# Kernel optimization log

Hardware: AMD Instinct MI355X
Metric: run time of the kernel (lower is better)

## Reference

```python
import jax, jax.numpy as jnp
import numpy as np

WINDOW = 512  # window_size from init_kwargs


def _sliding_window_attn(q, k, v, window):
    # q,k,v: [B, S, H, D]; each query attends to keys j with i-window < j <= i (causal band)
    B, S, H, D = q.shape
    W = window
    NB = S // W  # S chosen divisible by W
    qb = q.reshape(B, NB, W, H, D)
    kb = k.reshape(B, NB, W, H, D)
    vb = v.reshape(B, NB, W, H, D)
    # previous block of keys/values (zeros for block 0, masked out below)
    kprev = jnp.pad(kb, ((0, 0), (1, 0), (0, 0), (0, 0), (0, 0)))[:, :NB]
    vprev = jnp.pad(vb, ((0, 0), (1, 0), (0, 0), (0, 0), (0, 0)))[:, :NB]
    kcat = jnp.concatenate([kprev, kb], axis=2)  # [B, NB, 2W, H, D]
    vcat = jnp.concatenate([vprev, vb], axis=2)
    qi = jnp.arange(W)
    kj = jnp.arange(2 * W) - W  # key position relative to block start
    rel = kj[None, :] - qi[:, None]  # [W, 2W]
    win_mask = (rel <= 0) & (rel > -W)  # causal window of size W (incl. self)
    blk = jnp.arange(NB)
    valid_key = (blk[:, None, None] > 0) | (kj[None, None, :] >= 0)  # block 0 has no prev
    mask = win_mask[None] & valid_key  # [NB, W, 2W]
    scale = 1.0 / np.sqrt(D).astype(np.float32)
    scores = jnp.einsum('bnqhd,bnkhd->bhnqk', qb, kcat) * scale  # [B,H,NB,W,2W]
    scores = jnp.where(mask[None, None], scores, jnp.finfo(scores.dtype).min)
    probs = jax.nn.softmax(scores, axis=-1)
    out = jnp.einsum('bhnqk,bnkhd->bnqhd', probs, vcat)  # [B,NB,W,H,D]
    return out.reshape(B, S, H, D)


def setup_inputs() -> dict:
    B, S, H, D = 2, 8192, 8, 64
    root = jax.random.key(0)
    k1, k2, k3, k4, k5 = jax.random.split(root, 5)
    query = jax.random.normal(k1, (B, S, H, D), dtype=jnp.float32)
    key = jax.random.normal(k2, (B, S, H, D), dtype=jnp.float32)
    value = jax.random.normal(k3, (B, S, H, D), dtype=jnp.float32)
    W_out = jax.random.normal(k4, (H * D, H * D), dtype=jnp.float32) * (1.0 / np.sqrt(H * D))
    b_out = jax.random.normal(k5, (H * D,), dtype=jnp.float32) * 0.01
    return {'query': query, 'key': key, 'value': value, 'W_out': W_out, 'b_out': b_out}


def reference(query, key, value, W_out, b_out):
    B, S, H, D = query.shape
    # seq_len (8192) > window_size (512) -> sliding-window branch of the module
    attn = _sliding_window_attn(query, key, value, WINDOW)
    flat = attn.reshape(B, S, H * D)
    # out_proj (nn.Linear); dropout=0.0 is identity; no attention_mask
    return flat @ W_out.T + b_out
```

## Files before the change

### kernel.cpp

```cpp
#include <hip/hip_runtime.h>

#define B_ 2
#define S_ 8192
#define H_ 8
#define D_ 64
#define HD_ 512
#define WIN_ 512

typedef __bf16 bf16x8 __attribute__((ext_vector_type(8)));
typedef float f32x4 __attribute__((ext_vector_type(4)));
typedef unsigned short u16;
typedef unsigned int u32;

__device__ __forceinline__ u16 f2bf(float f) {
  u32 u = __float_as_uint(f);
  u += 0x7FFFu + ((u >> 16) & 1u);
  return (u16)(u >> 16);
}

__device__ __forceinline__ bf16x8 cvt8s(const float* p, float s) {
  const float4 a = *(const float4*)p;
  const float4 b = *(const float4*)(p + 4);
  union { u16 s[8]; bf16x8 v; } r;
  r.s[0] = f2bf(a.x * s); r.s[1] = f2bf(a.y * s); r.s[2] = f2bf(a.z * s); r.s[3] = f2bf(a.w * s);
  r.s[4] = f2bf(b.x * s); r.s[5] = f2bf(b.y * s); r.s[6] = f2bf(b.z * s); r.s[7] = f2bf(b.w * s);
  return r.v;
}

#define MFMA(a, b, c) __builtin_amdgcn_mfma_f32_16x16x32_bf16(a, b, c, 0, 0, 0)

__global__ __launch_bounds__(256) void cvt_kernel(const float* __restrict__ in,
                                                  u16* __restrict__ out, int n4) {
  int i = blockIdx.x * 256 + threadIdx.x;
  if (i < n4) {
    float4 f = ((const float4*)in)[i];
    ushort4 r;
    r.x = f2bf(f.x); r.y = f2bf(f.y); r.z = f2bf(f.z); r.w = f2bf(f.w);
    ((ushort4*)out)[i] = r;
  }
}

__global__ __launch_bounds__(1024, 4) void attn_kernel(const float* __restrict__ q,
                                                       const float* __restrict__ kf,
                                                       const float* __restrict__ vf,
                                                       u16* __restrict__ attn) {
  const int tid = threadIdx.x;
  const int lane = tid & 63;
  const int wave = tid >> 6;
  const int lg = lane >> 4;
  const int lj = lane & 15;
  const int bid = (int)blockIdx.x;
  const int swz = (bid & 7) * 64 + (bid >> 3);
  const int qc = swz & 31;
  const int bh = swz >> 5;
  const int b = bh >> 3, h = bh & 7;
  const int q0blk = qc * 256;
  const int q0w = q0blk + wave * 16;

  __shared__ __align__(16) u16 klds0[64 * 64], klds1[64 * 64];
  __shared__ __align__(16) u16 vlds0[64 * 64], vlds1[64 * 64];
  __shared__ __align__(16) u16 plds[16][16 * 40];

  const float qscale = 0.125f * 1.4426950408889634f;
  bf16x8 aq0, aq1;
  {
    const float* qrow = q + ((size_t)(b * S_ + q0w + lj) * H_ + h) * D_;
    aq0 = cvt8s(qrow + lg * 8, qscale);
    aq1 = cvt8s(qrow + 32 + lg * 8, qscale);
  }

  f32x4 o0 = {0.f, 0.f, 0.f, 0.f}, o1 = o0, o2 = o0, o3 = o0;
  float lacc[4] = {0.f, 0.f, 0.f, 0.f};

  const int tbw32 = (q0w >= WIN_) ? ((q0w - (WIN_ - 1)) >> 5) : 0;
  const int tew32 = (q0w + 15) >> 5;
  const bool wmask = (q0w >= WIN_);
  const int tbu = (q0blk >= WIN_) ? ((q0blk - (WIN_ - 1)) >> 6) : 0;
  const int teu = (q0blk + 255) >> 6;

  const bool isK = (tid < 256);
  const bool stager = (tid < 512);
  const float *gfA = nullptr, *gfB = nullptr;
  const size_t gstepf = (size_t)64 * H_ * D_;
  int dstA = 0, dstB = 0, vkey = 0, vd0 = 0;
  if (isK) {
    const int c = tid & 7;
    const int r0 = tid >> 3;
    const int r1 = r0 + 32;
    gfA = kf + ((size_t)(b * S_ + r0) * H_ + h) * D_ + c * 8;
    gfB = kf + ((size_t)(b * S_ + r1) * H_ + h) * D_ + c * 8;
    dstA = r0 * 64 + ((c * 8) ^ ((r0 & 7) << 3));
    dstB = r1 * 64 + ((c * 8) ^ ((r1 & 7) << 3));
  } else if (stager) {
    const int u = tid - 256;
    vkey = u & 63;
    vd0 = (u >> 6) * 8;
    gfA = vf + ((size_t)(b * S_ + vkey) * H_ + h) * D_ + vd0;
    gfB = gfA + 32;
  }

  auto kpack = [](float4 a, float4 c) {
    union { u16 s[8]; uint4 q; } t;
    t.s[0] = f2bf(a.x); t.s[1] = f2bf(a.y); t.s[2] = f2bf(a.z); t.s[3] = f2bf(a.w);
    t.s[4] = f2bf(c.x); t.s[5] = f2bf(c.y); t.s[6] = f2bf(c.z); t.s[7] = f2bf(c.w);
    return t.q;
  };
  auto vscatter = [&](u16* vb, int d0, float4 a, float4 c) {
    float vals[8] = {a.x, a.y, a.z, a.w, c.x, c.y, c.z, c.w};
#pragma unroll
    for (int i = 0; i < 8; ++i) {
      const int d = d0 + i;
      vb[d * 64 + (vkey ^ ((d & 7) << 3))] = f2bf(vals[i]);
    }
  };

  const int ko0 = lj * 64 + ((lg * 8) ^ ((lj & 7) << 3));
  const int ko1 = lj * 64 + ((32 + lg * 8) ^ ((lj & 7) << 3));
  const int po = lj * 40 + lg * 8;

  if (stager) {
    float4 a0 = *(const float4*)(gfA + gstepf * tbu);
    float4 b0 = *(const float4*)(gfA + gstepf * tbu + 4);
    float4 a1 = *(const float4*)(gfB + gstepf * tbu);
    float4 b1 = *(const float4*)(gfB + gstepf * tbu + 4);
    if (isK) {
      *(uint4*)(klds0 + dstA) = kpack(a0, b0);
      *(uint4*)(klds0 + dstB) = kpack(a1, b1);
    } else {
      vscatter(vlds0, vd0, a0, b0);
      vscatter(vlds0, vd0 + 32, a1, b1);
    }
  }
  float4 gaA, gbA, gaB, gbB;
  if (stager && tbu < teu) {
    gaA = *(const float4*)(gfA + gstepf * (tbu + 1));
    gbA = *(const float4*)(gfA + gstepf * (tbu + 1) + 4);
    gaB = *(const float4*)(gfB + gstepf * (tbu + 1));
    gbB = *(const float4*)(gfB + gstepf * (tbu + 1) + 4);
  }
  __syncthreads();

  int cur = 0;
  for (int t = tbu; t <= teu; ++t) {
    const u16* K = cur ? klds1 : klds0;
    const u16* V = cur ? vlds1 : vlds0;
#pragma unroll
    for (int s = 0; s < 2; ++s) {
      const int ts = t * 2 + s;
      if (ts >= tbw32 && ts <= tew32) {
        const u16* Kb = K + s * 2048;
        bf16x8 k00 = *(const bf16x8*)(Kb + ko0);
        bf16x8 k01 = *(const bf16x8*)(Kb + ko1);
        bf16x8 k10 = *(const bf16x8*)(Kb + ko0 + 1024);
        bf16x8 k11 = *(const bf16x8*)(Kb + ko1 + 1024);

        f32x4 sA = {0.f, 0.f, 0.f, 0.f}, sB = sA;
        sA = MFMA(aq0, k00, sA);
        sA = MFMA(aq1, k01, sA);
        sB = MFMA(aq0, k10, sB);
        sB = MFMA(aq1, k11, sB);

        const bool edge = (ts == tew32) || (wmask && ts == tbw32);
        const int kt = ts * 32;
        u16* ps = &plds[wave][0];
#pragma unroll
        for (int r = 0; r < 4; ++r) {
          float ea = __builtin_amdgcn_exp2f(sA[r]);
          float eb = __builtin_amdgcn_exp2f(sB[r]);
          if (edge) {
            const int qpos = q0w + lg * 4 + r;
            const int kA = kt + lj, kB = kA + 16;
            const bool okA = (kA <= qpos) && (kA > qpos - WIN_);
            const bool okB = (kB <= qpos) && (kB > qpos - WIN_);
            ea = okA ? ea : 0.f;
            eb = okB ? eb : 0.f;
          }
          lacc[r] += ea + eb;
          ps[(lg * 4 + r) * 40 + lj] = (u16)(__float_as_uint(ea) >> 16);
          ps[(lg * 4 + r) * 40 + 16 + lj] = (u16)(__float_as_uint(eb) >> 16);
        }
        bf16x8 ap = *(const bf16x8*)(ps + po);

        const int vos = lj * 64 + ((s * 32 + lg * 8) ^ ((lj & 7) << 3));
        bf16x8 v0 = *(const bf16x8*)(V + vos);
        bf16x8 v1 = *(const bf16x8*)(V + vos + 1024);
        bf16x8 v2 = *(const bf16x8*)(V + vos + 2048);
        bf16x8 v3 = *(const bf16x8*)(V + vos + 3072);
        o0 = MFMA(ap, v0, o0);
        o1 = MFMA(ap, v1, o1);
        o2 = MFMA(ap, v2, o2);
        o3 = MFMA(ap, v3, o3);
      }
    }

    if (stager && t < teu) {
      if (isK) {
        u16* dl = cur ? klds0 : klds1;
        *(uint4*)(dl + dstA) = kpack(gaA, gbA);
        *(uint4*)(dl + dstB) = kpack(gaB, gbB);
      } else {
        u16* vb = cur ? vlds0 : vlds1;
        vscatter(vb, vd0, gaA, gbA);
        vscatter(vb, vd0 + 32, gaB, gbB);
      }
    }
    __syncthreads();
    if (stager && t + 1 < teu) {
      gaA = *(const float4*)(gfA + gstepf * (t + 2));
      gbA = *(const float4*)(gfA + gstepf * (t + 2) + 4);
      gaB = *(const float4*)(gfB + gstepf * (t + 2));
      gbB = *(const float4*)(gfB + gstepf * (t + 2) + 4);
    }
    cur ^= 1;
  }

#pragma unroll
  for (int r = 0; r < 4; ++r) {
    float l = lacc[r];
    l += __shfl_xor(l, 1);
    l += __shfl_xor(l, 2);
    l += __shfl_xor(l, 4);
    l += __shfl_xor(l, 8);
    const float inv = 1.0f / l;
    const int row = q0w + lg * 4 + r;
    u16* orow = attn + (size_t)(b * S_ + row) * HD_ + h * D_;
    orow[lj] = f2bf(o0[r] * inv);
    orow[16 + lj] = f2bf(o1[r] * inv);
    orow[32 + lj] = f2bf(o2[r] * inv);
    orow[48 + lj] = f2bf(o3[r] * inv);
  }
}

__global__ __launch_bounds__(512) void gemm_kernel(const u16* __restrict__ A,
                                                   const u16* __restrict__ Wb,
                                                   const float* __restrict__ bias,
                                                   float* __restrict__ out) {
  const int tid = threadIdx.x;
  const int lane = tid & 63;
  const int wave = tid >> 6;
  const int lg = lane >> 4, lj = lane & 15;
  const int phys = (int)blockIdx.x;
  const int swz = (phys & 7) * 32 + (phys >> 3);
  const int rb = swz >> 1, cb = swz & 1;
  const int wr = wave >> 2, wc = wave & 3;
  const int row0 = rb * 128;
  const int col0 = cb * 256 + wc * 64;

  __shared__ __align__(16) u16 alds[2][128 * 64];

  const int srow = tid >> 3;
  const int skc = tid & 7;
  const u16* ag0 = A + (size_t)(row0 + srow) * HD_ + skc * 8;
  const u16* ag1 = A + (size_t)(row0 + 64 + srow) * HD_ + skc * 8;
  const int dst0 = srow * 64 + ((skc * 8) ^ ((srow & 7) << 3));
  const int dst1 = (64 + srow) * 64 + ((skc * 8) ^ ((srow & 7) << 3));

  f32x4 acc[4][4];
#pragma unroll
  for (int fr = 0; fr < 4; ++fr)
#pragma unroll
    for (int fc = 0; fc < 4; ++fc) acc[fr][fc] = (f32x4){0.f, 0.f, 0.f, 0.f};

  *(uint4*)(&alds[0][dst0]) = *(const uint4*)ag0;
  *(uint4*)(&alds[0][dst1]) = *(const uint4*)ag1;
  __syncthreads();

  uint4 pre0, pre1;
  int cur = 0;
  for (int kt = 0; kt < HD_; kt += 64) {
    if (kt + 64 < HD_) {
      pre0 = *(const uint4*)(ag0 + kt + 64);
      pre1 = *(const uint4*)(ag1 + kt + 64);
    }
    const u16* Abuf = alds[cur];
#pragma unroll
    for (int ks = 0; ks < 2; ++ks) {
      bf16x8 fa[4], fb[4];
#pragma unroll
      for (int fr = 0; fr < 4; ++fr) {
        const int rr = wr * 64 + fr * 16 + lj;
        fa[fr] = *(const bf16x8*)(Abuf + rr * 64 + ((ks * 32 + lg * 8) ^ ((lj & 7) << 3)));
      }
#pragma unroll
      for (int fc = 0; fc < 4; ++fc)
        fb[fc] = *(const bf16x8*)(Wb + (size_t)(col0 + fc * 16 + lj) * HD_ + kt + ks * 32 + lg * 8);
#pragma unroll
      for (int fr = 0; fr < 4; ++fr)
#pragma unroll
        for (int fc = 0; fc < 4; ++fc)
          acc[fr][fc] = MFMA(fa[fr], fb[fc], acc[fr][fc]);
    }
    if (kt + 64 < HD_) {
      u16* db = alds[cur ^ 1];
      *(uint4*)(&db[dst0]) = pre0;
      *(uint4*)(&db[dst1]) = pre1;
    }
    __syncthreads();
    cur ^= 1;
  }

#pragma unroll
  for (int fc = 0; fc < 4; ++fc) {
    const float bv = bias[col0 + fc * 16 + lj];
#pragma unroll
    for (int fr = 0; fr < 4; ++fr) {
#pragma unroll
      for (int r = 0; r < 4; ++r) {
        const int row = row0 + wr * 64 + fr * 16 + lg * 4 + r;
        out[(size_t)row * HD_ + col0 + fc * 16 + lj] = acc[fr][fc][r] + bv;
      }
    }
  }
}

extern "C" void kernel_launch(void* const* d_in, const int* in_sizes, int n_in,
                              void* d_out, int out_size, void* d_ws, size_t ws_size,
                              hipStream_t stream) {
  const float* q = (const float*)d_in[0];
  const float* k = (const float*)d_in[1];
  const float* v = (const float*)d_in[2];
  const float* w = (const float*)d_in[3];
  const float* bias = (const float*)d_in[4];
  float* out = (float*)d_out;

  char* ws = (char*)d_ws;
  u16* attn = (u16*)ws;
  u16* wb = (u16*)(ws + 16777216);

  hipLaunchKernelGGL(cvt_kernel, dim3(256), dim3(256), 0, stream, w, wb, 65536);
  hipLaunchKernelGGL(attn_kernel, dim3(512), dim3(1024), 0, stream, q, k, v, attn);
  hipLaunchKernelGGL(gemm_kernel, dim3(256), dim3(512), 0, stream, attn, wb, bias, out);
}
```

Baseline: 83.94 us.

## Process two 16-row query sub-tiles per wave to reuse K/V fragments

Each wave now handles 32 query rows as two 16-row sub-tiles, and each block covers 512 queries instead of 256, so the grid is halved. K and V fragments loaded from LDS are reused across both sub-tiles, which cuts LDS traffic and the global K/V staging per query. Costs are more registers per thread (two sets of accumulators and Q fragments), fewer blocks (256) to fill the GPU, and some extra wasted tiles at the window edges.

```diff
diff --git a/kernel.cpp b/kernel.cpp
--- a/kernel.cpp
+++ b/kernel.cpp
@@ -50,33 +50,44 @@
   const int lg = lane >> 4;
   const int lj = lane & 15;
   const int bid = (int)blockIdx.x;
-  const int swz = (bid & 7) * 64 + (bid >> 3);
-  const int qc = swz & 31;
-  const int bh = swz >> 5;
+  const int swz = (bid & 7) * 32 + (bid >> 3);
+  const int qc = swz & 15;
+  const int bh = swz >> 4;
   const int b = bh >> 3, h = bh & 7;
-  const int q0blk = qc * 256;
-  const int q0w = q0blk + wave * 16;
+  const int q0blk = qc * 512;
+  const int q0w = q0blk + wave * 32;
 
   __shared__ __align__(16) u16 klds0[64 * 64], klds1[64 * 64];
   __shared__ __align__(16) u16 vlds0[64 * 64], vlds1[64 * 64];
   __shared__ __align__(16) u16 plds[16][16 * 40];
 
   const float qscale = 0.125f * 1.4426950408889634f;
-  bf16x8 aq0, aq1;
-  {
-    const float* qrow = q + ((size_t)(b * S_ + q0w + lj) * H_ + h) * D_;
-    aq0 = cvt8s(qrow + lg * 8, qscale);
-    aq1 = cvt8s(qrow + 32 + lg * 8, qscale);
-  }
-
-  f32x4 o0 = {0.f, 0.f, 0.f, 0.f}, o1 = o0, o2 = o0, o3 = o0;
-  float lacc[4] = {0.f, 0.f, 0.f, 0.f};
-
-  const int tbw32 = (q0w >= WIN_) ? ((q0w - (WIN_ - 1)) >> 5) : 0;
-  const int tew32 = (q0w + 15) >> 5;
-  const bool wmask = (q0w >= WIN_);
+  bf16x8 aq[2][2];
+#pragma unroll
+  for (int qs = 0; qs < 2; ++qs) {
+    const float* qrow = q + ((size_t)(b * S_ + q0w + qs * 16 + lj) * H_ + h) * D_;
+    aq[qs][0] = cvt8s(qrow + lg * 8, qscale);
+    aq[qs][1] = cvt8s(qrow + 32 + lg * 8, qscale);
+  }
+
+  f32x4 o[2][4];
+#pragma unroll
+  for (int qs = 0; qs < 2; ++qs)
+#pragma unroll
+    for (int g = 0; g < 4; ++g) o[qs][g] = (f32x4){0.f, 0.f, 0.f, 0.f};
+  float lacc[2][4] = {};
+
+  const int ts_end = q0w >> 5;
+  int tbq[2];
+  bool wm[2];
+#pragma unroll
+  for (int qs = 0; qs < 2; ++qs) {
+    const int qq = q0w + qs * 16;
+    wm[qs] = (qq >= WIN_);
+    tbq[qs] = wm[qs] ? ((qq - (WIN_ - 1)) >> 5) : 0;
+  }
   const int tbu = (q0blk >= WIN_) ? ((q0blk - (WIN_ - 1)) >> 6) : 0;
-  const int teu = (q0blk + 255) >> 6;
+  const int teu = (q0blk + 511) >> 6;
 
   const bool isK = (tid < 256);
   const bool stager = (tid < 512);
@@ -147,49 +158,52 @@
 #pragma unroll
     for (int s = 0; s < 2; ++s) {
       const int ts = t * 2 + s;
-      if (ts >= tbw32 && ts <= tew32) {
+      if (ts >= tbq[0] && ts <= ts_end) {
         const u16* Kb = K + s * 2048;
         bf16x8 k00 = *(const bf16x8*)(Kb + ko0);
         bf16x8 k01 = *(const bf16x8*)(Kb + ko1);
         bf16x8 k10 = *(const bf16x8*)(Kb + ko0 + 1024);
         bf16x8 k11 = *(const bf16x8*)(Kb + ko1 + 1024);
-
-        f32x4 sA = {0.f, 0.f, 0.f, 0.f}, sB = sA;
-        sA = MFMA(aq0, k00, sA);
-        sA = MFMA(aq1, k01, sA);
-        sB = MFMA(aq0, k10, sB);
-        sB = MFMA(aq1, k11, sB);
-
-        const bool edge = (ts == tew32) || (wmask && ts == tbw32);
-        const int kt = ts * 32;
-        u16* ps = &plds[wave][0];
-#pragma unroll
-        for (int r = 0; r < 4; ++r) {
-          float ea = __builtin_amdgcn_exp2f(sA[r]);
-          float eb = __builtin_amdgcn_exp2f(sB[r]);
-          if (edge) {
-            const int qpos = q0w + lg * 4 + r;
-            const int kA = kt + lj, kB = kA + 16;
-            const bool okA = (kA <= qpos) && (kA > qpos - WIN_);
-            const bool okB = (kB <= qpos) && (kB > qpos - WIN_);
-            ea = okA ? ea : 0.f;
-            eb = okB ? eb : 0.f;
-          }
-          lacc[r] += ea + eb;
-          ps[(lg * 4 + r) * 40 + lj] = (u16)(__float_as_uint(ea) >> 16);
-          ps[(lg * 4 + r) * 40 + 16 + lj] = (u16)(__float_as_uint(eb) >> 16);
-        }
-        bf16x8 ap = *(const bf16x8*)(ps + po);
-
         const int vos = lj * 64 + ((s * 32 + lg * 8) ^ ((lj & 7) << 3));
         bf16x8 v0 = *(const bf16x8*)(V + vos);
         bf16x8 v1 = *(const bf16x8*)(V + vos + 1024);
         bf16x8 v2 = *(const bf16x8*)(V + vos + 2048);
         bf16x8 v3 = *(const bf16x8*)(V + vos + 3072);
-        o0 = MFMA(ap, v0, o0);
-        o1 = MFMA(ap, v1, o1);
-        o2 = MFMA(ap, v2, o2);
-        o3 = MFMA(ap, v3, o3);
+
+        const int kt = ts * 32;
+#pragma unroll
+        for (int qs = 0; qs < 2; ++qs) {
+          if (ts < tbq[qs]) continue;
+          f32x4 sA = {0.f, 0.f, 0.f, 0.f}, sB = sA;
+          sA = MFMA(aq[qs][0], k00, sA);
+          sA = MFMA(aq[qs][1], k01, sA);
+          sB = MFMA(aq[qs][0], k10, sB);
+          sB = MFMA(aq[qs][1], k11, sB);
+
+          const bool edge = (ts == ts_end) || (wm[qs] && ts == tbq[qs]);
+          u16* ps = &plds[wave][0];
+#pragma unroll
+          for (int r = 0; r < 4; ++r) {
+            float ea = __builtin_amdgcn_exp2f(sA[r]);
+            float eb = __builtin_amdgcn_exp2f(sB[r]);
+            if (edge) {
+              const int qpos = q0w + qs * 16 + lg * 4 + r;
+              const int kA = kt + lj, kB = kA + 16;
+              const bool okA = (kA <= qpos) && (kA > qpos - WIN_);
+              const bool okB = (kB <= qpos) && (kB > qpos - WIN_);
+              ea = okA ? ea : 0.f;
+              eb = okB ? eb : 0.f;
+            }
+            lacc[qs][r] += ea + eb;
+            ps[(lg * 4 + r) * 40 + lj] = (u16)(__float_as_uint(ea) >> 16);
+            ps[(lg * 4 + r) * 40 + 16 + lj] = (u16)(__float_as_uint(eb) >> 16);
+          }
+          bf16x8 ap = *(const bf16x8*)(ps + po);
+          o[qs][0] = MFMA(ap, v0, o[qs][0]);
+          o[qs][1] = MFMA(ap, v1, o[qs][1]);
+          o[qs][2] = MFMA(ap, v2, o[qs][2]);
+          o[qs][3] = MFMA(ap, v3, o[qs][3]);
+        }
       }
     }
 
@@ -215,19 +229,22 @@
   }
 
 #pragma unroll
-  for (int r = 0; r < 4; ++r) {
-    float l = lacc[r];
-    l += __shfl_xor(l, 1);
-    l += __shfl_xor(l, 2);
-    l += __shfl_xor(l, 4);
-    l += __shfl_xor(l, 8);
-    const float inv = 1.0f / l;
-    const int row = q0w + lg * 4 + r;
-    u16* orow = attn + (size_t)(b * S_ + row) * HD_ + h * D_;
-    orow[lj] = f2bf(o0[r] * inv);
-    orow[16 + lj] = f2bf(o1[r] * inv);
-    orow[32 + lj] = f2bf(o2[r] * inv);
-    orow[48 + lj] = f2bf(o3[r] * inv);
+  for (int qs = 0; qs < 2; ++qs) {
+#pragma unroll
+    for (int r = 0; r < 4; ++r) {
+      float l = lacc[qs][r];
+      l += __shfl_xor(l, 1);
+      l += __shfl_xor(l, 2);
+      l += __shfl_xor(l, 4);
+      l += __shfl_xor(l, 8);
+      const float inv = 1.0f / l;
+      const int row = q0w + qs * 16 + lg * 4 + r;
+      u16* orow = attn + (size_t)(b * S_ + row) * HD_ + h * D_;
+      orow[lj] = f2bf(o[qs][0][r] * inv);
+      orow[16 + lj] = f2bf(o[qs][1][r] * inv);
+      orow[32 + lj] = f2bf(o[qs][2][r] * inv);
+      orow[48 + lj] = f2bf(o[qs][3][r] * inv);
+    }
   }
 }
 
@@ -328,6 +345,6 @@
   u16* wb = (u16*)(ws + 16777216);
 
   hipLaunchKernelGGL(cvt_kernel, dim3(256), dim3(256), 0, stream, w, wb, 65536);
-  hipLaunchKernelGGL(attn_kernel, dim3(512), dim3(1024), 0, stream, q, k, v, attn);
+  hipLaunchKernelGGL(attn_kernel, dim3(256), dim3(1024), 0, stream, q, k, v, attn);
   hipLaunchKernelGGL(gemm_kernel, dim3(256), dim3(512), 0, stream, attn, wb, bias, out);
 }
```

Result: slower. 132.8 us (+58.2%).
